# Performance work log

Measured on AMD Instinct MI355X. Metric: run time of the kernel, lower is better.

Reference implementation:

```python
import jax, jax.numpy as jnp
import numpy as np

N = 20000
E = 160000
H = 8          # heads
D = 96         # head_dim (768 // 8)
C = H * D      # 768 hidden channels
G = 256        # num graphs
NUM_CLASSES = 32
SLOPE = 0.2    # GATv2 LeakyReLU negative slope


def layer_norm(x, w, b, eps=1e-5):
    mu = jnp.mean(x, axis=-1, keepdims=True)
    var = jnp.mean(jnp.square(x - mu), axis=-1, keepdims=True)
    return (x - mu) * jax.lax.rsqrt(var + eps) * w + b


def gatv2_layer(x, src, dst, Wl, bl, Wr, br, att, bias):
    # x: [N, C]; src/dst: [E'] with self loops included
    xl = (x @ Wl + bl).reshape(N, H, D)   # source projection
    xr = (x @ Wr + br).reshape(N, H, D)   # target projection
    e = xl[src] + xr[dst]                 # [E', H, D] edge gather
    e = jnp.where(e > 0, e, SLOPE * e)    # LeakyReLU
    logits = jnp.einsum('ehd,hd->eh', e, att)  # [E', H]
    m = jax.ops.segment_max(logits, dst, num_segments=N)
    ex = jnp.exp(logits - m[dst])
    s = jax.ops.segment_sum(ex, dst, num_segments=N)
    alpha = ex / s[dst]                   # segment softmax over in-edges
    out = jax.ops.segment_sum(alpha[:, :, None] * xl[src], dst, num_segments=N)
    return out.reshape(N, C) + bias


def setup_inputs() -> dict:
    key = jax.random.key(0)
    ks = jax.random.split(key, 24)
    x = jax.random.normal(ks[0], (N, 768), jnp.float32)
    edge_index = jax.random.randint(ks[1], (2, E), 0, N, jnp.int64)
    batch = jnp.sort(jax.random.randint(ks[2], (N,), 0, G, jnp.int64))
    sc = 1.0 / np.sqrt(C)
    p = {
        'x': x, 'edge_index': edge_index, 'batch': batch,
        'w_in': jax.random.normal(ks[3], (768, C), jnp.float32) * sc,
        'b_in': jnp.zeros((C,), jnp.float32),
        'Wl': jax.random.normal(ks[4], (3, C, C), jnp.float32) * sc,
        'bl': jnp.zeros((3, C), jnp.float32),
        'Wr': jax.random.normal(ks[5], (3, C, C), jnp.float32) * sc,
        'br': jnp.zeros((3, C), jnp.float32),
        'att': jax.random.normal(ks[6], (3, H, D), jnp.float32) * (1.0 / np.sqrt(D)),
        'gat_bias': jnp.zeros((3, C), jnp.float32),
        'ln_w': jnp.ones((3, C), jnp.float32),
        'ln_b': jnp.zeros((3, C), jnp.float32),
        'out_ln_w': jnp.ones((3 * C,), jnp.float32),
        'out_ln_b': jnp.zeros((3 * C,), jnp.float32),
        'w_out': jax.random.normal(ks[7], (3 * C, NUM_CLASSES), jnp.float32) * (1.0 / np.sqrt(3 * C)),
        'b_out': jnp.zeros((NUM_CLASSES,), jnp.float32),
    }
    return p


def reference(x, edge_index, batch, w_in, b_in, Wl, bl, Wr, br, att, gat_bias,
              ln_w, ln_b, out_ln_w, out_ln_b, w_out, b_out):
    # add self loops (PyG add_self_loops=True)
    loops = jnp.arange(N, dtype=edge_index.dtype)
    src = jnp.concatenate([edge_index[0], loops])
    dst = jnp.concatenate([edge_index[1], loops])

    h = x @ w_in + b_in
    jumps = []
    for l in range(3):
        a = gatv2_layer(h, src, dst, Wl[l], bl[l], Wr[l], br[l], att[l], gat_bias[l])
        h = layer_norm(a + h, ln_w[l], ln_b[l])
        h = jax.nn.gelu(h, approximate=False)
        jumps.append(h)
    hc = jnp.concatenate(jumps, axis=-1)  # JumpingKnowledge 'cat' -> [N, 3C]

    # global mean pool over graphs
    sums = jax.ops.segment_sum(hc, batch, num_segments=G)
    cnt = jax.ops.segment_sum(jnp.ones((N, 1), hc.dtype), batch, num_segments=G)
    pooled = sums / jnp.maximum(cnt, 1.0)

    out = layer_norm(pooled, out_ln_w, out_ln_b)
    return out @ w_out + b_out
```

## Files before the change

kernel.cpp:

```cpp
#include <hip/hip_runtime.h>

#define N_NODES 20000
#define N_EDGES 160000
#define CH      768
#define CH3     2304
#define NGRAPH  256
#define NCLS    32

typedef __bf16 bf16v8 __attribute__((ext_vector_type(8)));
typedef float  f32x4  __attribute__((ext_vector_type(4)));

__device__ __forceinline__ float b2f(ushort u) {
    union { float f; unsigned u; } x; x.u = ((unsigned)u) << 16; return x.f;
}
__device__ __forceinline__ ushort f2b(float f) {
    union { float f; unsigned u; } x; x.f = f;
    unsigned r = x.u + 0x7FFFu + ((x.u >> 16) & 1u);
    return (ushort)(r >> 16);
}
__device__ __forceinline__ void load12(const ushort* __restrict__ p, float* o) {
    const ushort4* q = (const ushort4*)p;
    ushort4 a = q[0], b = q[1], c = q[2];
    o[0]=b2f(a.x); o[1]=b2f(a.y); o[2]=b2f(a.z); o[3]=b2f(a.w);
    o[4]=b2f(b.x); o[5]=b2f(b.y); o[6]=b2f(b.z); o[7]=b2f(b.w);
    o[8]=b2f(c.x); o[9]=b2f(c.y); o[10]=b2f(c.z); o[11]=b2f(c.w);
}
__device__ __forceinline__ void load12f(const float* __restrict__ p, float* o) {
    const float4* q = (const float4*)p;
    float4 a = q[0], b = q[1], c = q[2];
    o[0]=a.x; o[1]=a.y; o[2]=a.z; o[3]=a.w;
    o[4]=b.x; o[5]=b.y; o[6]=b.z; o[7]=b.w;
    o[8]=c.x; o[9]=c.y; o[10]=c.z; o[11]=c.w;
}
__device__ __forceinline__ void async_copy16(void* lds, const void* gp) {
    __builtin_amdgcn_global_load_lds((const void __attribute__((address_space(1)))*)gp,
                                     (void __attribute__((address_space(3)))*)lds, 16, 0, 0);
}

__global__ void cvt_x_kernel(const float* __restrict__ src, ushort* __restrict__ dst, int n4) {
    int i = blockIdx.x * 256 + threadIdx.x;
    if (i >= n4) return;
    float4 v = ((const float4*)src)[i];
    ushort4 o; o.x = f2b(v.x); o.y = f2b(v.y); o.z = f2b(v.z); o.w = f2b(v.w);
    ((ushort4*)dst)[i] = o;
}

__global__ void transpose_cvt_all(const float* __restrict__ w_in,
                                  const float* __restrict__ Wl,
                                  const float* __restrict__ Wr,
                                  ushort* __restrict__ wt_in,
                                  ushort* __restrict__ wt_l) {
    __shared__ float tile[32][33];
    int z = blockIdx.z;
    const float* in;
    ushort* out;
    if (z == 0) { in = w_in; out = wt_in; }
    else {
        int l = (z - 1) >> 1, isr = (z - 1) & 1;
        in  = (isr ? Wr : Wl) + (size_t)l * CH * CH;
        out = wt_l + (size_t)l * 1536 * CH + (size_t)isr * CH * CH;
    }
    int bx = blockIdx.x * 32, by = blockIdx.y * 32;
    int tx = threadIdx.x, ty = threadIdx.y;
    #pragma unroll
    for (int i = ty; i < 32; i += 8) tile[i][tx] = in[(size_t)(by + i) * CH + bx + tx];
    __syncthreads();
    #pragma unroll
    for (int i = ty; i < 32; i += 8) out[(size_t)(bx + i) * CH + by + tx] = f2b(tile[tx][i]);
}

__global__ void count_both_kernel(const int* __restrict__ dst, int* __restrict__ deg, int e,
                                  const int* __restrict__ batch, int* __restrict__ gcount, int n) {
    int i = blockIdx.x * 256 + threadIdx.x;
    if (i < e) atomicAdd(&deg[dst[i]], 1);
    if (i < n) { atomicAdd(&deg[i], 1); atomicAdd(&gcount[batch[i]], 1); }
}
__global__ __launch_bounds__(1024) void scan_kernel(const int* __restrict__ deg,
                                                    int* __restrict__ rowptr, int n) {
    __shared__ int part[1024];
    int t = threadIdx.x;
    const int chunk = (n + 1023) / 1024;
    int base = t * chunk;
    int s = 0;
    for (int i = 0; i < chunk; ++i) { int idx = base + i; if (idx < n) s += deg[idx]; }
    part[t] = s; __syncthreads();
    for (int off = 1; off < 1024; off <<= 1) {
        int v = (t >= off) ? part[t - off] : 0;
        __syncthreads();
        part[t] += v;
        __syncthreads();
    }
    int run = (t == 0) ? 0 : part[t - 1];
    for (int i = 0; i < chunk; ++i) {
        int idx = base + i;
        if (idx < n) { rowptr[idx] = run; run += deg[idx]; }
    }
    if (t == 1023) rowptr[n] = part[1023];
}
__global__ void selfloop_kernel(const int* __restrict__ rowptr, int* __restrict__ csrc,
                                int* __restrict__ cursor, int n) {
    int i = blockIdx.x * 256 + threadIdx.x;
    if (i < n) { int p = rowptr[i]; csrc[p] = i; cursor[i] = p + 1; }
}
__global__ void scatter_kernel(const int* __restrict__ src, const int* __restrict__ dst,
                               int* __restrict__ cursor, int* __restrict__ csrc, int e) {
    int i = blockIdx.x * 256 + threadIdx.x;
    if (i < e) { int p = atomicAdd(&cursor[dst[i]], 1); csrc[p] = src[i]; }
}
__global__ __launch_bounds__(256) void gscan_kernel(const int* __restrict__ gcount,
                                                    int* __restrict__ gstart) {
    __shared__ int p[256];
    int t = threadIdx.x;
    p[t] = gcount[t]; __syncthreads();
    for (int off = 1; off < 256; off <<= 1) {
        int v = (t >= off) ? p[t - off] : 0;
        __syncthreads();
        p[t] += v;
        __syncthreads();
    }
    gstart[t] = p[t] - gcount[t];
    if (t == 255) gstart[256] = p[255];
}

__global__ __launch_bounds__(256) void gemm_bf16_kernel(
    const ushort* __restrict__ A, int lda,
    const ushort* __restrict__ Bt,
    const float* __restrict__ biasA, const float* __restrict__ biasB, int nsplit,
    ushort* __restrict__ C, int ldc, int M) {
    __shared__ __bf16 As[128 * 32];
    __shared__ __bf16 Bs[128 * 32];
    int tid = threadIdx.x;
    int wave = tid >> 6, lane = tid & 63;
    int wr = wave >> 1, wc = wave & 1;

    int bid = blockIdx.y * gridDim.x + blockIdx.x;
    int pf = 8 * gridDim.y;
    int p  = bid / pf;
    int rem = bid - p * pf;
    int rp = min(8, (int)gridDim.x - p * 8);
    int row_t = p * 8 + rem % rp;
    int col_t = rem / rp;
    int row0 = row_t * 128, col0 = col_t * 128;

    int c1 = wave * 64 + lane, c2 = c1 + 256;
    int ar1 = min(row0 + (c1 >> 2), M - 1), ak1 = (c1 & 3) * 8;
    int ar2 = min(row0 + (c2 >> 2), M - 1), ak2 = (c2 & 3) * 8;
    int br1 = col0 + (c1 >> 2), br2 = col0 + (c2 >> 2);
    const ushort* a1 = A + (size_t)ar1 * lda + ak1;
    const ushort* a2 = A + (size_t)ar2 * lda + ak2;
    const ushort* b1 = Bt + (size_t)br1 * CH + ak1;
    const ushort* b2 = Bt + (size_t)br2 * CH + ak2;
    __bf16* asb1 = As + (wave * 64) * 8;
    __bf16* asb2 = As + (256 + wave * 64) * 8;
    __bf16* bsb1 = Bs + (wave * 64) * 8;
    __bf16* bsb2 = Bs + (256 + wave * 64) * 8;

    f32x4 acc[4][4] = {};
    int l16 = lane & 15, lq = lane >> 4;

    for (int k0 = 0; k0 < CH; k0 += 32) {
        async_copy16(asb1, a1 + k0);
        async_copy16(asb2, a2 + k0);
        async_copy16(bsb1, b1 + k0);
        async_copy16(bsb2, b2 + k0);
        __syncthreads();
        bf16v8 av[4], bv[4];
        #pragma unroll
        for (int i = 0; i < 4; ++i)
            av[i] = *(const bf16v8*)(As + ((wr * 64 + i * 16 + l16) * 32 + lq * 8));
        #pragma unroll
        for (int j = 0; j < 4; ++j)
            bv[j] = *(const bf16v8*)(Bs + ((wc * 64 + j * 16 + l16) * 32 + lq * 8));
        #pragma unroll
        for (int i = 0; i < 4; ++i)
            #pragma unroll
            for (int j = 0; j < 4; ++j)
                acc[i][j] = __builtin_amdgcn_mfma_f32_16x16x32_bf16(av[i], bv[j], acc[i][j], 0, 0, 0);
        __syncthreads();
    }
    #pragma unroll
    for (int i = 0; i < 4; ++i) {
        int mbase = row0 + wr * 64 + i * 16 + lq * 4;
        #pragma unroll
        for (int j = 0; j < 4; ++j) {
            int col = col0 + wc * 64 + j * 16 + l16;
            float bb = (col < nsplit) ? biasA[col] : biasB[col - nsplit];
            #pragma unroll
            for (int r = 0; r < 4; ++r) {
                int mm = mbase + r;
                if (mm < M) C[(size_t)mm * ldc + col] = f2b(acc[i][j][r] + bb);
            }
        }
    }
}

__global__ __launch_bounds__(256) void gat_node_kernel(
    const ushort* __restrict__ xlxr,
    const ushort* __restrict__ hin, int ldh,
    const int* __restrict__ rowptr, const int* __restrict__ csrc,
    const float* __restrict__ att, const float* __restrict__ gbias,
    const float* __restrict__ lnw, const float* __restrict__ lnb,
    ushort* __restrict__ hout, int nn) {
    int wv = threadIdx.x >> 6, lane = threadIdx.x & 63;
    int n = blockIdx.x * 4 + wv;
    int c0 = lane * 12;
    const ushort* __restrict__ xbase = xlxr + c0;
    float attv[12], xr[12], acc1[12] = {}, acc2[12] = {};
    load12f(att + c0, attv);
    load12(xbase + (size_t)n * 1536 + CH, xr);
    float s1 = 0.f, s2 = 0.f;
    int rs = rowptr[n], re = rowptr[n + 1];
    int e = rs;
    for (; e + 1 < re; e += 2) {
        int sa = csrc[e], sb = csrc[e + 1];
        float xa[12], xb[12];
        load12(xbase + (size_t)sa * 1536, xa);
        load12(xbase + (size_t)sb * 1536, xb);
        float da = 0.f, db = 0.f;
        #pragma unroll
        for (int j = 0; j < 12; ++j) {
            float va = xa[j] + xr[j]; va = fmaxf(va, 0.2f * va);
            float vb = xb[j] + xr[j]; vb = fmaxf(vb, 0.2f * vb);
            da = fmaf(va, attv[j], da);
            db = fmaf(vb, attv[j], db);
        }
        da += __shfl_xor(da, 1); db += __shfl_xor(db, 1);
        da += __shfl_xor(da, 2); db += __shfl_xor(db, 2);
        da += __shfl_xor(da, 4); db += __shfl_xor(db, 4);
        float ea = __expf(da), eb = __expf(db);
        s1 += ea; s2 += eb;
        #pragma unroll
        for (int j = 0; j < 12; ++j) {
            acc1[j] = fmaf(ea, xa[j], acc1[j]);
            acc2[j] = fmaf(eb, xb[j], acc2[j]);
        }
    }
    if (e < re) {
        int sa = csrc[e];
        float xa[12];
        load12(xbase + (size_t)sa * 1536, xa);
        float da = 0.f;
        #pragma unroll
        for (int j = 0; j < 12; ++j) {
            float va = xa[j] + xr[j]; va = fmaxf(va, 0.2f * va);
            da = fmaf(va, attv[j], da);
        }
        da += __shfl_xor(da, 1);
        da += __shfl_xor(da, 2);
        da += __shfl_xor(da, 4);
        float ea = __expf(da);
        s1 += ea;
        #pragma unroll
        for (int j = 0; j < 12; ++j) acc1[j] = fmaf(ea, xa[j], acc1[j]);
    }
    float inv = 1.f / (s1 + s2);
    float hres[12], gb[12], tv[12];
    load12(hin + (size_t)n * ldh + c0, hres);
    load12f(gbias + c0, gb);
    float lsum = 0.f, lsq = 0.f;
    #pragma unroll
    for (int j = 0; j < 12; ++j) {
        tv[j] = (acc1[j] + acc2[j]) * inv + gb[j] + hres[j];
        lsum += tv[j];
        lsq = fmaf(tv[j], tv[j], lsq);
    }
    #pragma unroll
    for (int o = 1; o < 64; o <<= 1) { lsum += __shfl_xor(lsum, o); lsq += __shfl_xor(lsq, o); }
    float mu = lsum * (1.f / 768.f);
    float var = lsq * (1.f / 768.f) - mu * mu;
    float rstd = rsqrtf(var + 1e-5f);
    float wv12[12], bv12[12];
    load12f(lnw + c0, wv12);
    load12f(lnb + c0, bv12);
    ushort* op = hout + (size_t)n * CH3 + c0;
    ushort4 u[3];
    #pragma unroll
    for (int k = 0; k < 3; ++k) {
        float g[4];
        #pragma unroll
        for (int q = 0; q < 4; ++q) {
            int j = k * 4 + q;
            float y = (tv[j] - mu) * rstd * wv12[j] + bv12[j];
            g[q] = 0.5f * y * (1.f + erff(y * 0.70710678118f));
        }
        u[k].x = f2b(g[0]); u[k].y = f2b(g[1]); u[k].z = f2b(g[2]); u[k].w = f2b(g[3]);
        ((ushort4*)op)[k] = u[k];
    }
}

__global__ __launch_bounds__(256) void pool_kernel(const ushort* __restrict__ hc,
                                                   const int* __restrict__ gstart,
                                                   float* __restrict__ pooled) {
    int g = blockIdx.x;
    int c = blockIdx.y * 256 + threadIdx.x;
    int s = gstart[g], e = gstart[g + 1];
    const ushort* p = hc + (size_t)s * CH3 + c;
    float a0 = 0.f, a1 = 0.f, a2 = 0.f, a3 = 0.f;
    int n = s;
    for (; n + 3 < e; n += 4) {
        a0 += b2f(p[0]);
        a1 += b2f(p[CH3]);
        a2 += b2f(p[2 * CH3]);
        a3 += b2f(p[3 * CH3]);
        p += 4 * CH3;
    }
    for (; n < e; ++n) { a0 += b2f(*p); p += CH3; }
    float a = (a0 + a1) + (a2 + a3);
    pooled[(size_t)g * CH3 + c] = a * (1.f / (float)max(e - s, 1));
}

__global__ __launch_bounds__(256) void head_kernel(const float* __restrict__ pooled,
                                                   const float* __restrict__ olnw,
                                                   const float* __restrict__ olnb,
                                                   const float* __restrict__ wout,
                                                   const float* __restrict__ bout,
                                                   float* __restrict__ outp) {
    __shared__ float row[CH3];
    __shared__ float red[8];
    __shared__ float parts[8][32];
    int g = blockIdx.x, t = threadIdx.x;
    int lane = t & 63, wv = t >> 6;
    float s = 0.f;
    for (int c = t; c < CH3; c += 256) { float v = pooled[(size_t)g * CH3 + c]; row[c] = v; s += v; }
    #pragma unroll
    for (int o = 1; o < 64; o <<= 1) s += __shfl_xor(s, o);
    if (lane == 0) red[wv] = s;
    __syncthreads();
    float mu = (red[0] + red[1] + red[2] + red[3]) * (1.f / (float)CH3);
    float q = 0.f;
    for (int c = t; c < CH3; c += 256) { float d = row[c] - mu; q += d * d; }
    #pragma unroll
    for (int o = 1; o < 64; o <<= 1) q += __shfl_xor(q, o);
    if (lane == 0) red[4 + wv] = q;
    __syncthreads();
    float rstd = rsqrtf((red[4] + red[5] + red[6] + red[7]) * (1.f / (float)CH3) + 1e-5f);
    for (int c = t; c < CH3; c += 256)
        row[c] = (row[c] - mu) * rstd * olnw[c] + olnb[c];
    __syncthreads();
    int j = t & 31, slice = t >> 5;
    float a = 0.f;
    int cb = slice * (CH3 / 8);
    for (int c = cb; c < cb + CH3 / 8; ++c) a += row[c] * wout[(size_t)c * 32 + j];
    parts[slice][j] = a;
    __syncthreads();
    if (t < 32) {
        float r = bout[t];
        #pragma unroll
        for (int si = 0; si < 8; ++si) r += parts[si][t];
        outp[(size_t)g * 32 + t] = r;
    }
}

extern "C" void kernel_launch(void* const* d_in, const int* in_sizes, int n_in,
                              void* d_out, int out_size, void* d_ws, size_t ws_size,
                              hipStream_t stream) {
    const float* x     = (const float*)d_in[0];
    const int*   ei    = (const int*)d_in[1];
    const int*   batch = (const int*)d_in[2];
    const float* w_in  = (const float*)d_in[3];
    const float* b_in  = (const float*)d_in[4];
    const float* Wl    = (const float*)d_in[5];
    const float* bl    = (const float*)d_in[6];
    const float* Wr    = (const float*)d_in[7];
    const float* br    = (const float*)d_in[8];
    const float* att   = (const float*)d_in[9];
    const float* gbias = (const float*)d_in[10];
    const float* lnw   = (const float*)d_in[11];
    const float* lnb   = (const float*)d_in[12];
    const float* olnw  = (const float*)d_in[13];
    const float* olnb  = (const float*)d_in[14];
    const float* wout  = (const float*)d_in[15];
    const float* bout  = (const float*)d_in[16];

    char* ws = (char*)d_ws;
    size_t off = 0;
    auto alloc = [&](size_t bytes) -> void* {
        void* p = ws + off;
        off = (off + bytes + 255) & ~(size_t)255;
        return p;
    };
    ushort* h0     = (ushort*)alloc((size_t)N_NODES * CH * 2);
    ushort* hc     = (ushort*)alloc((size_t)N_NODES * CH3 * 2);
    ushort* xlxr   = (ushort*)alloc((size_t)N_NODES * 1536 * 2);
    ushort* wt_in  = (ushort*)alloc((size_t)CH * CH * 2);
    ushort* wt_l   = (ushort*)alloc((size_t)3 * 1536 * CH * 2);
    int*    deg    = (int*)alloc((size_t)N_NODES * 4);
    int*    rowptr = (int*)alloc((size_t)(N_NODES + 1) * 4);
    int*    cursor = (int*)alloc((size_t)N_NODES * 4);
    int*    csrc   = (int*)alloc((size_t)(N_EDGES + N_NODES) * 4);
    int*    gcount = (int*)alloc(256 * 4);
    int*    gstart = (int*)alloc(257 * 4);
    float*  pooled = (float*)alloc((size_t)NGRAPH * CH3 * 4);
    if (off > ws_size) return;

    ushort* xc = hc;

    cvt_x_kernel<<<(N_NODES * CH / 4 + 255) / 256, 256, 0, stream>>>(x, xc, N_NODES * CH / 4);
    transpose_cvt_all<<<dim3(24, 24, 7), dim3(32, 8), 0, stream>>>(w_in, Wl, Wr, wt_in, wt_l);

    int nb = (N_NODES + 255) / 256, eb = (N_EDGES + 255) / 256;
    hipMemsetAsync(deg, 0, (size_t)N_NODES * 4, stream);
    hipMemsetAsync(gcount, 0, 256 * 4, stream);
    count_both_kernel<<<eb, 256, 0, stream>>>(ei + N_EDGES, deg, N_EDGES, batch, gcount, N_NODES);
    scan_kernel<<<1, 1024, 0, stream>>>(deg, rowptr, N_NODES);
    selfloop_kernel<<<nb, 256, 0, stream>>>(rowptr, csrc, cursor, N_NODES);
    scatter_kernel<<<eb, 256, 0, stream>>>(ei, ei + N_EDGES, cursor, csrc, N_EDGES);
    gscan_kernel<<<1, 256, 0, stream>>>(gcount, gstart);

    gemm_bf16_kernel<<<dim3(157, 6), 256, 0, stream>>>(
        xc, CH, wt_in, b_in, b_in, CH, h0, CH, N_NODES);

    for (int l = 0; l < 3; ++l) {
        const ushort* hprev = (l == 0) ? h0 : (hc + (size_t)(l - 1) * CH);
        int ldh = (l == 0) ? CH : CH3;
        gemm_bf16_kernel<<<dim3(157, 12), 256, 0, stream>>>(
            hprev, ldh, wt_l + (size_t)l * 1536 * CH,
            bl + (size_t)l * CH, br + (size_t)l * CH, CH,
            xlxr, 1536, N_NODES);
        gat_node_kernel<<<N_NODES / 4, 256, 0, stream>>>(
            xlxr, hprev, ldh, rowptr, csrc,
            att + (size_t)l * CH, gbias + (size_t)l * CH,
            lnw + (size_t)l * CH, lnb + (size_t)l * CH,
            hc + (size_t)l * CH, N_NODES);
    }

    pool_kernel<<<dim3(NGRAPH, CH3 / 256), 256, 0, stream>>>(hc, gstart, pooled);
    head_kernel<<<NGRAPH, 256, 0, stream>>>(pooled, olnw, olnb, wout, bout, (float*)d_out);
}
```

Measured before the change: 714.0 us.

## Double-buffer GEMM LDS tiles and XOR-swizzle K chunks against bank conflicts

The bf16 MFMA GEMM now uses two LDS buffers per operand, so the async copy of the next K-slice is issued before the current slice is computed. This replaces the previous single-buffer load, sync, compute, sync pattern and lets global loads overlap MFMA work. It also XOR-swizzles the 8-element K chunk position by row, on both the global source offset and the LDS read offset, to reduce LDS bank conflicts on the fragment loads. LDS use doubles, which may lower occupancy, and correctness relies on the async copy completing by the next barrier.

```diff
diff --git a/kernel.cpp b/kernel.cpp
--- a/kernel.cpp
+++ b/kernel.cpp
@@ -127,8 +127,8 @@
     const ushort* __restrict__ Bt,
     const float* __restrict__ biasA, const float* __restrict__ biasB, int nsplit,
     ushort* __restrict__ C, int ldc, int M) {
-    __shared__ __bf16 As[128 * 32];
-    __shared__ __bf16 Bs[128 * 32];
+    __shared__ __bf16 As[2][128 * 32];
+    __shared__ __bf16 Bs[2][128 * 32];
     int tid = threadIdx.x;
     int wave = tid >> 6, lane = tid & 63;
     int wr = wave >> 1, wc = wave & 1;
@@ -143,34 +143,44 @@
     int row0 = row_t * 128, col0 = col_t * 128;
 
     int c1 = wave * 64 + lane, c2 = c1 + 256;
-    int ar1 = min(row0 + (c1 >> 2), M - 1), ak1 = (c1 & 3) * 8;
-    int ar2 = min(row0 + (c2 >> 2), M - 1), ak2 = (c2 & 3) * 8;
+    int ak1 = ((c1 & 3) ^ ((c1 >> 3) & 3)) * 8;
+    int ak2 = ((c2 & 3) ^ ((c2 >> 3) & 3)) * 8;
+    int ar1 = min(row0 + (c1 >> 2), M - 1);
+    int ar2 = min(row0 + (c2 >> 2), M - 1);
     int br1 = col0 + (c1 >> 2), br2 = col0 + (c2 >> 2);
     const ushort* a1 = A + (size_t)ar1 * lda + ak1;
     const ushort* a2 = A + (size_t)ar2 * lda + ak2;
     const ushort* b1 = Bt + (size_t)br1 * CH + ak1;
     const ushort* b2 = Bt + (size_t)br2 * CH + ak2;
-    __bf16* asb1 = As + (wave * 64) * 8;
-    __bf16* asb2 = As + (256 + wave * 64) * 8;
-    __bf16* bsb1 = Bs + (wave * 64) * 8;
-    __bf16* bsb2 = Bs + (256 + wave * 64) * 8;
+    int wo1 = (wave * 64) * 8, wo2 = (256 + wave * 64) * 8;
 
     f32x4 acc[4][4] = {};
     int l16 = lane & 15, lq = lane >> 4;
-
-    for (int k0 = 0; k0 < CH; k0 += 32) {
-        async_copy16(asb1, a1 + k0);
-        async_copy16(asb2, a2 + k0);
-        async_copy16(bsb1, b1 + k0);
-        async_copy16(bsb2, b2 + k0);
-        __syncthreads();
+    int koff = (lq ^ ((l16 >> 1) & 3)) * 8;
+
+    async_copy16(As[0] + wo1, a1);
+    async_copy16(As[0] + wo2, a2);
+    async_copy16(Bs[0] + wo1, b1);
+    async_copy16(Bs[0] + wo2, b2);
+    __syncthreads();
+
+    #pragma unroll 2
+    for (int t = 0; t < 24; ++t) {
+        int cur = t & 1, nxt = cur ^ 1;
+        if (t < 23) {
+            int k0 = (t + 1) * 32;
+            async_copy16(As[nxt] + wo1, a1 + k0);
+            async_copy16(As[nxt] + wo2, a2 + k0);
+            async_copy16(Bs[nxt] + wo1, b1 + k0);
+            async_copy16(Bs[nxt] + wo2, b2 + k0);
+        }
         bf16v8 av[4], bv[4];
         #pragma unroll
         for (int i = 0; i < 4; ++i)
-            av[i] = *(const bf16v8*)(As + ((wr * 64 + i * 16 + l16) * 32 + lq * 8));
+            av[i] = *(const bf16v8*)(&As[cur][(wr * 64 + i * 16 + l16) * 32 + koff]);
         #pragma unroll
         for (int j = 0; j < 4; ++j)
-            bv[j] = *(const bf16v8*)(Bs + ((wc * 64 + j * 16 + l16) * 32 + lq * 8));
+            bv[j] = *(const bf16v8*)(&Bs[cur][(wc * 64 + j * 16 + l16) * 32 + koff]);
         #pragma unroll
         for (int i = 0; i < 4; ++i)
             #pragma unroll
@@ -178,6 +188,7 @@
                 acc[i][j] = __builtin_amdgcn_mfma_f32_16x16x32_bf16(av[i], bv[j], acc[i][j], 0, 0, 0);
         __syncthreads();
     }
+
     #pragma unroll
     for (int i = 0; i < 4; ++i) {
         int mbase = row0 + wr * 64 + i * 16 + lq * 4;
```

Result: no change. 720.1 us (+0.8%).

## Rewrite bf16 GEMM with 256x256 tiles, 4-stage async pipeline, swizzled LDS

Applied to the files above, without the earlier changes.

Replaces the 128x128 single-buffered GEMM with a 512-thread, 256x256-tile kernel that uses a 4-deep ring of LDS buffers fed by async copies, so global loads for later k-steps overlap with MFMA work. LDS columns are XOR-swizzled to reduce bank conflicts, wave priority is raised around MFMA bursts, and workgroups are remapped so that consecutive tiles land on the same XCD for L2 reuse. It needs more LDS and registers per block, and with only 237 or 474 blocks on a large GPU the number of blocks per CU may drop.

```diff
diff --git a/kernel.cpp b/kernel.cpp
--- a/kernel.cpp
+++ b/kernel.cpp
@@ -122,73 +122,110 @@
     if (t == 255) gstart[256] = p[255];
 }
 
-__global__ __launch_bounds__(256) void gemm_bf16_kernel(
+__global__ __launch_bounds__(512, 2) void gemm8_bf16_kernel(
     const ushort* __restrict__ A, int lda,
     const ushort* __restrict__ Bt,
     const float* __restrict__ biasA, const float* __restrict__ biasB, int nsplit,
-    ushort* __restrict__ C, int ldc, int M) {
-    __shared__ __bf16 As[128 * 32];
-    __shared__ __bf16 Bs[128 * 32];
+    ushort* __restrict__ C, int ldc, int M, int ncolt) {
+    __shared__ __bf16 As[4][256 * 32];
+    __shared__ __bf16 Bs[4][256 * 32];
     int tid = threadIdx.x;
-    int wave = tid >> 6, lane = tid & 63;
-    int wr = wave >> 1, wc = wave & 1;
-
-    int bid = blockIdx.y * gridDim.x + blockIdx.x;
-    int pf = 8 * gridDim.y;
-    int p  = bid / pf;
-    int rem = bid - p * pf;
-    int rp = min(8, (int)gridDim.x - p * 8);
-    int row_t = p * 8 + rem % rp;
-    int col_t = rem / rp;
-    int row0 = row_t * 128, col0 = col_t * 128;
-
-    int c1 = wave * 64 + lane, c2 = c1 + 256;
-    int ar1 = min(row0 + (c1 >> 2), M - 1), ak1 = (c1 & 3) * 8;
-    int ar2 = min(row0 + (c2 >> 2), M - 1), ak2 = (c2 & 3) * 8;
-    int br1 = col0 + (c1 >> 2), br2 = col0 + (c2 >> 2);
-    const ushort* a1 = A + (size_t)ar1 * lda + ak1;
-    const ushort* a2 = A + (size_t)ar2 * lda + ak2;
-    const ushort* b1 = Bt + (size_t)br1 * CH + ak1;
-    const ushort* b2 = Bt + (size_t)br2 * CH + ak2;
-    __bf16* asb1 = As + (wave * 64) * 8;
-    __bf16* asb2 = As + (256 + wave * 64) * 8;
-    __bf16* bsb1 = Bs + (wave * 64) * 8;
-    __bf16* bsb2 = Bs + (256 + wave * 64) * 8;
-
-    f32x4 acc[4][4] = {};
+    int wid = tid >> 6, lane = tid & 63;
+    int wm = wid >> 2, wn = wid & 3;
     int l16 = lane & 15, lq = lane >> 4;
 
-    for (int k0 = 0; k0 < CH; k0 += 32) {
-        async_copy16(asb1, a1 + k0);
-        async_copy16(asb2, a2 + k0);
-        async_copy16(bsb1, b1 + k0);
-        async_copy16(bsb2, b2 + k0);
-        __syncthreads();
+    int nwg = gridDim.x, bid = blockIdx.x;
+    int q = nwg >> 3, rm = nwg & 7;
+    int xcd = bid & 7, idx = bid >> 3;
+    int wg = (xcd < rm ? xcd * (q + 1) : rm * (q + 1) + (xcd - rm) * q) + idx;
+    int row_t = wg / ncolt, col_t = wg - row_t * ncolt;
+    int row0 = row_t * 256, col0 = col_t * 256;
+
+    int s1 = 512 + tid;
+    int r0 = tid >> 2, r1 = s1 >> 2;
+    int ac0 = ((tid & 3) ^ ((tid >> 3) & 3)) * 8;
+    int ac1 = ((s1 & 3) ^ ((s1 >> 3) & 3)) * 8;
+    const ushort* pa0 = A + (size_t)min(row0 + r0, M - 1) * lda + ac0;
+    const ushort* pa1 = A + (size_t)min(row0 + r1, M - 1) * lda + ac1;
+    const ushort* pb0 = Bt + (size_t)(col0 + r0) * CH + ac0;
+    const ushort* pb1 = Bt + (size_t)(col0 + r1) * CH + ac1;
+    int wb0 = (wid * 64) * 8, wb1 = (512 + wid * 64) * 8;
+
+    int koffE = (lq ^ ((l16 >> 1) & 3)) * 8;
+
+    f32x4 acc[8][4] = {};
+
+    #define STAGE_A(buf, t) do { int k0 = (t) * 32;                   \
+        async_copy16(&As[buf][wb0], pa0 + k0);                        \
+        async_copy16(&As[buf][wb1], pa1 + k0); } while (0)
+    #define STAGE_B(buf, t) do { int k0 = (t) * 32;                   \
+        async_copy16(&Bs[buf][wb0], pb0 + k0);                        \
+        async_copy16(&Bs[buf][wb1], pb1 + k0); } while (0)
+
+    STAGE_A(0, 0); STAGE_B(0, 0);
+    STAGE_A(1, 1); STAGE_B(1, 1);
+    STAGE_A(2, 2); STAGE_B(2, 2);
+    asm volatile("s_waitcnt vmcnt(8)" ::: "memory");
+    __builtin_amdgcn_s_barrier();
+
+    for (int t = 0; t < 24; ++t) {
+        int buf = t & 3, sbuf = (t + 3) & 3;
+        const __bf16* Ab = &As[buf][(wm * 128 + l16) * 32 + koffE];
+        const __bf16* Bb = &Bs[buf][(wn * 64 + l16) * 32 + koffE];
         bf16v8 av[4], bv[4];
         #pragma unroll
-        for (int i = 0; i < 4; ++i)
-            av[i] = *(const bf16v8*)(As + ((wr * 64 + i * 16 + l16) * 32 + lq * 8));
-        #pragma unroll
-        for (int j = 0; j < 4; ++j)
-            bv[j] = *(const bf16v8*)(Bs + ((wc * 64 + j * 16 + l16) * 32 + lq * 8));
-        #pragma unroll
-        for (int i = 0; i < 4; ++i)
+        for (int f = 0; f < 4; ++f) av[f] = *(const bf16v8*)(Ab + f * 16 * 32);
+        #pragma unroll
+        for (int g = 0; g < 4; ++g) bv[g] = *(const bf16v8*)(Bb + g * 16 * 32);
+        if (t < 21) STAGE_A(sbuf, t + 3);
+        __builtin_amdgcn_s_barrier();
+        asm volatile("s_waitcnt lgkmcnt(0)" ::: "memory");
+        __builtin_amdgcn_sched_barrier(0);
+        __builtin_amdgcn_s_setprio(1);
+        #pragma unroll
+        for (int f = 0; f < 4; ++f)
             #pragma unroll
-            for (int j = 0; j < 4; ++j)
-                acc[i][j] = __builtin_amdgcn_mfma_f32_16x16x32_bf16(av[i], bv[j], acc[i][j], 0, 0, 0);
-        __syncthreads();
-    }
-    #pragma unroll
-    for (int i = 0; i < 4; ++i) {
-        int mbase = row0 + wr * 64 + i * 16 + lq * 4;
-        #pragma unroll
-        for (int j = 0; j < 4; ++j) {
-            int col = col0 + wc * 64 + j * 16 + l16;
-            float bb = (col < nsplit) ? biasA[col] : biasB[col - nsplit];
+            for (int g = 0; g < 4; ++g)
+                acc[f][g] = __builtin_amdgcn_mfma_f32_16x16x32_bf16(av[f], bv[g], acc[f][g], 0, 0, 0);
+        __builtin_amdgcn_s_setprio(0);
+        __builtin_amdgcn_s_barrier();
+        #pragma unroll
+        for (int f = 0; f < 4; ++f) av[f] = *(const bf16v8*)(Ab + (64 + f * 16) * 32);
+        if (t < 21) STAGE_B(sbuf, t + 3);
+        __builtin_amdgcn_s_barrier();
+        asm volatile("s_waitcnt lgkmcnt(0)" ::: "memory");
+        __builtin_amdgcn_sched_barrier(0);
+        __builtin_amdgcn_s_setprio(1);
+        #pragma unroll
+        for (int f = 0; f < 4; ++f)
+            #pragma unroll
+            for (int g = 0; g < 4; ++g)
+                acc[4 + f][g] = __builtin_amdgcn_mfma_f32_16x16x32_bf16(av[f], bv[g], acc[4 + f][g], 0, 0, 0);
+        __builtin_amdgcn_s_setprio(0);
+        if (t < 21)       { asm volatile("s_waitcnt vmcnt(8)" ::: "memory"); }
+        else if (t == 21) { asm volatile("s_waitcnt vmcnt(4)" ::: "memory"); }
+        else if (t == 22) { asm volatile("s_waitcnt vmcnt(0)" ::: "memory"); }
+        __builtin_amdgcn_s_barrier();
+    }
+    #undef STAGE_A
+    #undef STAGE_B
+
+    float bias[4];
+    #pragma unroll
+    for (int g = 0; g < 4; ++g) {
+        int col = col0 + wn * 64 + g * 16 + l16;
+        bias[g] = (col < nsplit) ? biasA[col] : biasB[col - nsplit];
+    }
+    #pragma unroll
+    for (int f = 0; f < 8; ++f) {
+        int mbase = row0 + wm * 128 + f * 16 + lq * 4;
+        #pragma unroll
+        for (int g = 0; g < 4; ++g) {
+            int col = col0 + wn * 64 + g * 16 + l16;
             #pragma unroll
             for (int r = 0; r < 4; ++r) {
                 int mm = mbase + r;
-                if (mm < M) C[(size_t)mm * ldc + col] = f2b(acc[i][j][r] + bb);
+                if (mm < M) C[(size_t)mm * ldc + col] = f2b(acc[f][g][r] + bias[g]);
             }
         }
     }
@@ -407,16 +444,16 @@
     scatter_kernel<<<eb, 256, 0, stream>>>(ei, ei + N_EDGES, cursor, csrc, N_EDGES);
     gscan_kernel<<<1, 256, 0, stream>>>(gcount, gstart);
 
-    gemm_bf16_kernel<<<dim3(157, 6), 256, 0, stream>>>(
-        xc, CH, wt_in, b_in, b_in, CH, h0, CH, N_NODES);
+    gemm8_bf16_kernel<<<79 * 3, 512, 0, stream>>>(
+        xc, CH, wt_in, b_in, b_in, CH, h0, CH, N_NODES, 3);
 
     for (int l = 0; l < 3; ++l) {
         const ushort* hprev = (l == 0) ? h0 : (hc + (size_t)(l - 1) * CH);
         int ldh = (l == 0) ? CH : CH3;
-        gemm_bf16_kernel<<<dim3(157, 12), 256, 0, stream>>>(
+        gemm8_bf16_kernel<<<79 * 6, 512, 0, stream>>>(
             hprev, ldh, wt_l + (size_t)l * 1536 * CH,
             bl + (size_t)l * CH, br + (size_t)l * CH, CH,
-            xlxr, 1536, N_NODES);
+            xlxr, 1536, N_NODES, 6);
         gat_node_kernel<<<N_NODES / 4, 256, 0, stream>>>(
             xlxr, hprev, ldh, rowptr, csrc,
             att + (size_t)l * CH, gbias + (size_t)l * CH,
```

Measured after the change: 725.4 us. About the same (+1.6%).
